# Optimization experiments

Hardware: AMD Instinct MI355X
Metric: run time of the kernel (lower is better)

The kernel has to match this reference:

```python
import jax, jax.numpy as jnp
import numpy as np
from jax import lax

NUM_CAMERAS = 15
INPUT_SIZE = 1024
NUM_TIMESTEPS = 60
BATCH = 256


def setup_inputs() -> dict:
    key = jax.random.key(0)
    k1, k2, k3, k4, k5, k6 = jax.random.split(key, 6)
    H = INPUT_SIZE
    s = 1.0 / np.sqrt(H)  # PyTorch RNNCell init: U(-1/sqrt(H), 1/sqrt(H))
    x = jax.random.normal(k1, (BATCH, H), dtype=jnp.float32)
    cam = jax.random.randint(k2, (BATCH,), 0, NUM_CAMERAS)
    # per-camera GRUCell params, PyTorch layout: gates [r, z, n] stacked -> 3H
    W_ih = jax.random.uniform(k3, (NUM_CAMERAS, 3 * H, H), jnp.float32, -s, s)
    W_hh = jax.random.uniform(k4, (NUM_CAMERAS, 3 * H, H), jnp.float32, -s, s)
    b_ih = jax.random.uniform(k5, (NUM_CAMERAS, 3 * H), jnp.float32, -s, s)
    b_hh = jax.random.uniform(k6, (NUM_CAMERAS, 3 * H), jnp.float32, -s, s)
    return {"x": x, "cam": cam, "W_ih": W_ih, "W_hh": W_hh, "b_ih": b_ih, "b_hh": b_hh}


def reference(x, cam, W_ih, W_hh, b_ih, b_hh):
    B, H = x.shape
    rows = jnp.arange(B)
    # input projection is constant across timesteps (same x fed every step):
    # compute for all cameras as one GEMM, then gather each sample's camera.
    gi_all = jnp.einsum('bh,cgh->bcg', x, W_ih) + b_ih[None]  # [B,C,3H]
    gi = gi_all[rows, cam]                                     # [B,3H]
    gi_r, gi_z, gi_n = jnp.split(gi, 3, axis=1)
    bhh = b_hh[cam]                                            # [B,3H]

    def step(h, _):
        gh_all = jnp.einsum('bh,cgh->bcg', h, W_hh)            # [B,C,3H] GEMM
        gh = gh_all[rows, cam] + bhh                           # [B,3H]
        gh_r, gh_z, gh_n = jnp.split(gh, 3, axis=1)
        r = jax.nn.sigmoid(gi_r + gh_r)
        z = jax.nn.sigmoid(gi_z + gh_z)
        n = jnp.tanh(gi_n + r * gh_n)
        h_new = (1.0 - z) * n + z * h
        return h_new, h_new

    h0 = jnp.zeros((B, H), dtype=x.dtype)
    _, hs = lax.scan(step, h0, None, length=NUM_TIMESTEPS)     # [T,B,H]
    return jnp.transpose(hs, (1, 2, 0))                        # [B,H,T]
```

## Files before the change

### kernel.cpp

```cpp
#include <hip/hip_runtime.h>
#include <math.h>

#define HD 1024
#define BB 256
#define NCAM 15
#define TT 60
#define G3 3072
#define LDW 36
#define NS 24
#define TCH 20

typedef short bf16x8 __attribute__((ext_vector_type(8)));
typedef _Float16 f16x8 __attribute__((ext_vector_type(8)));
typedef float f32x4 __attribute__((ext_vector_type(4)));

__device__ __forceinline__ unsigned short f2h(float f) {
    _Float16 h = (_Float16)f;
    unsigned short u;
    __builtin_memcpy(&u, &h, 2);
    return u;
}
__device__ __forceinline__ float sigf(float v) { return 1.f / (1.f + expf(-v)); }

__device__ __forceinline__ void dma16(const void* g, void* l) {
    __builtin_amdgcn_global_load_lds(
        (const __attribute__((address_space(1))) unsigned int*)g,
        (__attribute__((address_space(3))) unsigned int*)l, 16, 0, 0);
}

__global__ void group_kernel(const int* __restrict__ cam,
                             int* __restrict__ off, int* __restrict__ list) {
    __shared__ int cnt[NCAM];
    __shared__ int soff[NCAM + 1];
    int tid = threadIdx.x;
    if (tid < NCAM) cnt[tid] = 0;
    __syncthreads();
    int c = cam[tid];
    int pos = atomicAdd(&cnt[c], 1);
    __syncthreads();
    if (tid == 0) {
        soff[0] = 0;
        for (int i = 0; i < NCAM; ++i) soff[i + 1] = soff[i] + cnt[i];
    }
    __syncthreads();
    list[soff[c] + pos] = tid;
    if (tid <= NCAM) off[tid] = soff[tid];
}

__global__ __launch_bounds__(256) void gi_gemm_kernel(
    const float* __restrict__ W_ih, const float* __restrict__ b_ih,
    const float* __restrict__ b_hh, const float* __restrict__ x,
    const int* __restrict__ off, const int* __restrict__ list,
    float* __restrict__ gi) {
    int c  = blockIdx.x;
    int r0 = blockIdx.y * 96;
    int tid = threadIdx.x;
    int tx = tid & 7, ty = tid >> 3;

    __shared__ __align__(16) float wlds[96 * LDW];
    __shared__ __align__(16) float hlds[NS * LDW];
    __shared__ int slist[NS];

    int base = off[c];
    int nc = off[c + 1] - base;

    for (int s0 = 0; s0 < nc; s0 += NS) {
        __syncthreads();
        if (tid < NS) slist[tid] = (s0 + tid < nc) ? list[base + s0 + tid] : -1;
        __syncthreads();

        float acc[3][3];
#pragma unroll
        for (int g = 0; g < 3; ++g)
#pragma unroll
            for (int q = 0; q < 3; ++q) acc[g][q] = 0.f;

        for (int k0 = 0; k0 < HD; k0 += 32) {
#pragma unroll
            for (int i = 0; i < 3; ++i) {
                int idx = tid + 256 * i;
                int row = idx >> 3, col4 = idx & 7;
                float4 w = *(const float4*)(W_ih +
                    ((size_t)c * G3 + r0 + row) * HD + k0 + col4 * 4);
                *(float4*)(wlds + row * LDW + col4 * 4) = w;
            }
            {
                int s = tid >> 3, col4 = tid & 7;
                if (s < NS) {
                    int b = slist[s];
                    float4 hv = make_float4(0.f, 0.f, 0.f, 0.f);
                    if (b >= 0)
                        hv = *(const float4*)(x + (size_t)b * HD + k0 + col4 * 4);
                    *(float4*)(hlds + s * LDW + col4 * 4) = hv;
                }
            }
            __syncthreads();
#pragma unroll
            for (int kk = 0; kk < 32; kk += 4) {
                float4 w0 = *(const float4*)(wlds + (0 * 32 + ty) * LDW + kk);
                float4 w1 = *(const float4*)(wlds + (1 * 32 + ty) * LDW + kk);
                float4 w2 = *(const float4*)(wlds + (2 * 32 + ty) * LDW + kk);
#pragma unroll
                for (int q = 0; q < 3; ++q) {
                    float4 hv = *(const float4*)(hlds + (tx + 8 * q) * LDW + kk);
                    acc[0][q] += w0.x * hv.x + w0.y * hv.y + w0.z * hv.z + w0.w * hv.w;
                    acc[1][q] += w1.x * hv.x + w1.y * hv.y + w1.z * hv.z + w1.w * hv.w;
                    acc[2][q] += w2.x * hv.x + w2.y * hv.y + w2.z * hv.z + w2.w * hv.w;
                }
            }
            __syncthreads();
        }
#pragma unroll
        for (int q = 0; q < 3; ++q) {
            int b = slist[tx + 8 * q];
            if (b >= 0) {
#pragma unroll
                for (int g = 0; g < 3; ++g) {
                    int R = r0 + g * 32 + ty;
                    float bias = b_ih[c * G3 + R];
                    if (R < 2 * HD) bias += b_hh[c * G3 + R];
                    gi[(size_t)b * G3 + R] = acc[g][q] + bias;
                }
            }
        }
    }
}

__global__ __launch_bounds__(256) void prep_kernel(
    const float* __restrict__ W_hh, unsigned short* __restrict__ Wimg) {
    int c = blockIdx.z, jt = blockIdx.y;
    int lin = blockIdx.x * 256 + threadIdx.x;
    int it  = lin / 768;
    int rem = lin - it * 768;
    int r = rem >> 3, kcp = rem & 7;
    int gate = r >> 5, jl = r & 31;
    int kc = kcp ^ (r & 7);
    int k = it * 64 + kc * 8;
    const float* src = W_hh + ((size_t)c * G3 + gate * HD + jt * 32 + jl) * HD + k;
    float4 v0 = *(const float4*)src;
    float4 v1 = *(const float4*)(src + 4);
    float v[8] = {v0.x, v0.y, v0.z, v0.w, v1.x, v1.y, v1.z, v1.w};
    unsigned int hp[4];
#pragma unroll
    for (int e = 0; e < 4; ++e) {
        unsigned short h0 = f2h(v[2 * e]), h1 = f2h(v[2 * e + 1]);
        hp[e] = (unsigned)h0 | ((unsigned)h1 << 16);
    }
    unsigned short* dst = Wimg + ((size_t)(c * 32 + jt) * 16 + it) * 6144 + r * 64 + kcp * 8;
    *(uint4*)dst = make_uint4(hp[0], hp[1], hp[2], hp[3]);
}

__global__ __launch_bounds__(128) void step_dma_kernel(
    const unsigned short* __restrict__ Wimg, const float* __restrict__ b_hh,
    const float* __restrict__ gi, const int* __restrict__ off,
    const int* __restrict__ list, const float* __restrict__ h_in,
    const unsigned short* __restrict__ hf_in, const unsigned short* __restrict__ hzero,
    float* __restrict__ h_out, unsigned short* __restrict__ hf_out) {
    int c  = blockIdx.x;
    int jt = blockIdx.y;
    int j0 = jt * 32;
    int tid = threadIdx.x;
    int lane = tid & 63;
    int w = tid >> 6;
    int l15 = lane & 15;
    int l4  = lane >> 4;

    __shared__ __align__(16) unsigned short Ash[2][6144];
    __shared__ __align__(16) unsigned short Bsh[2][2048];
    __shared__ int slist[32];

    const unsigned short* wbase = Wimg + (size_t)(c * 32 + jt) * 16 * 6144;
    int base = off[c];
    int nc = off[c + 1] - base;

    int bs[2], bkc[2];
#pragma unroll
    for (int i = 0; i < 2; ++i) {
        int p = i * 128 + tid;
        bs[i]  = p >> 3;
        bkc[i] = (p & 7) ^ (bs[i] & 7);
    }

    for (int s0 = 0; s0 < nc; s0 += 32) {
        __syncthreads();
        if (tid < 32) slist[tid] = (s0 + tid < nc) ? list[base + s0 + tid] : -1;
        __syncthreads();
        int rem = nc - s0;
        int nq = (rem > 16) ? 2 : 1;

        const unsigned short* bg[2];
        int bstep[2];
#pragma unroll
        for (int i = 0; i < 2; ++i) {
            int b = slist[bs[i]];
            bg[i] = (b >= 0) ? hf_in + (size_t)b * HD + bkc[i] * 8 : hzero;
            bstep[i] = (b >= 0) ? 1 : 0;
        }

        f32x4 acc[3][2];
#pragma unroll
        for (int g = 0; g < 3; ++g)
#pragma unroll
            for (int q = 0; q < 2; ++q) acc[g][q] = (f32x4){0.f, 0.f, 0.f, 0.f};

#define STAGE(NB, IT) do {                                                        \
        const char* asrc_ = (const char*)(wbase + (size_t)(IT) * 6144);           \
        _Pragma("unroll")                                                         \
        for (int i_ = 0; i_ < 6; ++i_)                                            \
            dma16(asrc_ + (i_ * 128 + tid) * 16,                                  \
                  (char*)(Ash[NB]) + (i_ * 128 + (w << 6)) * 16);                 \
        int k0_ = (IT) * 64;                                                      \
        _Pragma("unroll")                                                         \
        for (int i_ = 0; i_ < 2; ++i_)                                            \
            dma16(bg[i_] + k0_ * bstep[i_],                                       \
                  (char*)(Bsh[NB]) + (i_ * 128 + (w << 6)) * 16);                 \
    } while (0)

        STAGE(0, 0);
        asm volatile("s_waitcnt vmcnt(0)" ::: "memory");
        __builtin_amdgcn_s_barrier();

#pragma unroll 2
        for (int it = 0; it < 16; ++it) {
            int cur = it & 1;
            if (it < 15) STAGE(cur ^ 1, it + 1);

            const unsigned short* Acur = Ash[cur];
            const unsigned short* Bcur = Bsh[cur];
#pragma unroll
            for (int kt = 0; kt < 2; ++kt) {
                int kc = kt * 4 + l4;
                f16x8 bq[2];
#pragma unroll
                for (int q = 0; q < 2; ++q) {
                    if (q < nq) {
                        int s = q * 16 + l15;
                        int boff = s * 64 + ((kc ^ (s & 7)) * 8);
                        bq[q] = *(const f16x8*)(&Bcur[boff]);
                    }
                }
#pragma unroll
                for (int g = 0; g < 3; ++g) {
                    int r = g * 32 + w * 16 + l15;
                    int aoff = r * 64 + ((kc ^ (r & 7)) * 8);
                    f16x8 av = *(const f16x8*)(&Acur[aoff]);
#pragma unroll
                    for (int q = 0; q < 2; ++q) {
                        if (q < nq) {
                            acc[g][q] = __builtin_amdgcn_mfma_f32_16x16x32_f16(av, bq[q], acc[g][q], 0, 0, 0);
                        }
                    }
                }
            }
            if (it < 15) {
                asm volatile("s_waitcnt vmcnt(0)" ::: "memory");
                __builtin_amdgcn_s_barrier();
            }
        }
#undef STAGE

        int j = j0 + w * 16 + l4 * 4;
        f32x4 bhn = *(const f32x4*)(b_hh + c * G3 + 2 * HD + j);
#pragma unroll
        for (int q = 0; q < 2; ++q) {
            if (q < nq) {
                int b = slist[q * 16 + l15];
                if (b >= 0) {
                    const float* gib = gi + (size_t)b * G3;
                    f32x4 gr = *(const f32x4*)(gib + j);
                    f32x4 gz = *(const f32x4*)(gib + HD + j);
                    f32x4 gn = *(const f32x4*)(gib + 2 * HD + j);
                    f32x4 hp = *(const f32x4*)(h_in + (size_t)b * HD + j);
                    f32x4 hn;
#pragma unroll
                    for (int e = 0; e < 4; ++e) {
                        float r = sigf(gr[e] + acc[0][q][e]);
                        float z = sigf(gz[e] + acc[1][q][e]);
                        float n = tanhf(gn[e] + r * (acc[2][q][e] + bhn[e]));
                        hn[e] = (1.f - z) * n + z * hp[e];
                    }
                    unsigned int hw[2];
#pragma unroll
                    for (int e = 0; e < 2; ++e) {
                        unsigned short h0 = f2h(hn[2 * e]), h1 = f2h(hn[2 * e + 1]);
                        hw[e] = (unsigned)h0 | ((unsigned)h1 << 16);
                    }
                    *(f32x4*)(h_out + (size_t)b * HD + j) = hn;
                    *(uint2*)(hf_out + (size_t)b * HD + j) = make_uint2(hw[0], hw[1]);
                }
            }
        }
    }
}

__global__ __launch_bounds__(256) void tr_kernel(
    const float* __restrict__ ring, float* __restrict__ out, int t0) {
    int r = blockIdx.x * 256 + threadIdx.x;
    float v[TCH];
#pragma unroll
    for (int tt = 0; tt < TCH; ++tt)
        v[tt] = ring[(size_t)tt * (BB * HD) + r];
    float* dst = out + (size_t)r * TT + t0;
#pragma unroll
    for (int e = 0; e < TCH / 4; ++e)
        *(f32x4*)(dst + 4 * e) = (f32x4){v[4 * e], v[4 * e + 1], v[4 * e + 2], v[4 * e + 3]};
}

extern "C" void kernel_launch(void* const* d_in, const int* in_sizes, int n_in,
                              void* d_out, int out_size, void* d_ws, size_t ws_size,
                              hipStream_t stream) {
    const float* x    = (const float*)d_in[0];
    const int*   cam  = (const int*)d_in[1];
    const float* W_ih = (const float*)d_in[2];
    const float* W_hh = (const float*)d_in[3];
    const float* b_ih = (const float*)d_in[4];
    const float* b_hh = (const float*)d_in[5];
    float* out = (float*)d_out;

    char* ws = (char*)d_ws;
    int*   off   = (int*)ws;
    int*   list  = (int*)(ws + 64);
    unsigned short* hzero = (unsigned short*)(ws + 2048);
    float* gi    = (float*)(ws + 4096);
    float* hZ    = (float*)(ws + 3149824);
    unsigned short* hfA = (unsigned short*)(ws + 4198400);
    unsigned short* hfB = (unsigned short*)(ws + 4722688);
    float* ring  = (float*)(ws + 5246976);
    unsigned short* Wimg = (unsigned short*)(ws + 26218496);

    group_kernel<<<1, 256, 0, stream>>>(cam, off, list);
    gi_gemm_kernel<<<dim3(NCAM, G3 / 96), 256, 0, stream>>>(
        W_ih, b_ih, b_hh, x, off, list, gi);
    prep_kernel<<<dim3(48, 32, NCAM), 256, 0, stream>>>(W_hh, Wimg);
    hipMemsetAsync(hzero, 0, 2048, stream);
    hipMemsetAsync(hZ, 0, (size_t)BB * HD * sizeof(float), stream);
    hipMemsetAsync(hfA, 0, (size_t)BB * HD * sizeof(short), stream);

    const float* hin = hZ;
    const unsigned short* hf_in = hfA;
    unsigned short* hf_out = hfB;
    for (int t = 0; t < TT; ++t) {
        float* ringplane = ring + (size_t)(t % TCH) * BB * HD;
        step_dma_kernel<<<dim3(NCAM, HD / 32), 128, 0, stream>>>(
            Wimg, b_hh, gi, off, list, hin, hf_in, hzero,
            ringplane, hf_out);
        hin = ringplane;
        { const unsigned short* tmp = hf_in; hf_in = hf_out; hf_out = (unsigned short*)tmp; }
        if ((t % TCH) == TCH - 1)
            tr_kernel<<<BB * HD / 256, 256, 0, stream>>>(ring, out, t - (TCH - 1));
    }
}
```

Baseline: 1.817 ms.

## Deepen step kernel DMA pipeline to four LDS stages with partial waits

The per-step GRU GEMM kernel moves from double-buffered LDS staging with a full vmcnt(0) drain each iteration to a 4-buffer ring with three tiles in flight. Each iteration waits only on the oldest tile's loads via partial vmcnt counts. The sample list is now kept in registers and broadcast with __shfl instead of going through shared memory, which removes one barrier per chunk. In exchange, LDS per block doubles, which may lower occupancy, and the hand-tuned vmcnt counts must exactly match the number of issued DMA ops.

Measured after the change: 1.743 ms. 1.04x faster.

```diff
diff --git a/kernel.cpp b/kernel.cpp
--- a/kernel.cpp
+++ b/kernel.cpp
@@ -10,7 +10,6 @@
 #define NS 24
 #define TCH 20
 
-typedef short bf16x8 __attribute__((ext_vector_type(8)));
 typedef _Float16 f16x8 __attribute__((ext_vector_type(8)));
 typedef float f32x4 __attribute__((ext_vector_type(4)));
 
@@ -165,9 +164,8 @@
     int l15 = lane & 15;
     int l4  = lane >> 4;
 
-    __shared__ __align__(16) unsigned short Ash[2][6144];
-    __shared__ __align__(16) unsigned short Bsh[2][2048];
-    __shared__ int slist[32];
+    __shared__ __align__(16) unsigned short Ash[4][6144];
+    __shared__ __align__(16) unsigned short Bsh[4][2048];
 
     const unsigned short* wbase = Wimg + (size_t)(c * 32 + jt) * 16 * 6144;
     int base = off[c];
@@ -181,10 +179,27 @@
         bkc[i] = (p & 7) ^ (bs[i] & 7);
     }
 
+#define STG_A(NB, IT) do {                                                    \
+        const char* asrc_ = (const char*)(wbase + (size_t)(IT) * 6144);       \
+        _Pragma("unroll")                                                     \
+        for (int i_ = 0; i_ < 6; ++i_)                                        \
+            dma16(asrc_ + (i_ * 128 + tid) * 16,                              \
+                  (char*)(Ash[NB]) + (i_ * 128 + (w << 6)) * 16);             \
+    } while (0)
+#define STG_B(NB, IT) do {                                                    \
+        int k0_ = (IT) * 64;                                                  \
+        _Pragma("unroll")                                                     \
+        for (int i_ = 0; i_ < 2; ++i_)                                        \
+            dma16(bg[i_] + k0_ * bstep[i_],                                   \
+                  (char*)(Bsh[NB]) + (i_ * 128 + (w << 6)) * 16);             \
+    } while (0)
+
     for (int s0 = 0; s0 < nc; s0 += 32) {
         __syncthreads();
-        if (tid < 32) slist[tid] = (s0 + tid < nc) ? list[base + s0 + tid] : -1;
-        __syncthreads();
+
+        int sv = -1;
+        if (lane < 32) sv = (s0 + lane < nc) ? list[base + s0 + lane] : -1;
+
         int rem = nc - s0;
         int nq = (rem > 16) ? 2 : 1;
 
@@ -192,7 +207,7 @@
         int bstep[2];
 #pragma unroll
         for (int i = 0; i < 2; ++i) {
-            int b = slist[bs[i]];
+            int b = __shfl(sv, bs[i]);
             bg[i] = (b >= 0) ? hf_in + (size_t)b * HD + bkc[i] * 8 : hzero;
             bstep[i] = (b >= 0) ? 1 : 0;
         }
@@ -203,30 +218,22 @@
 #pragma unroll
             for (int q = 0; q < 2; ++q) acc[g][q] = (f32x4){0.f, 0.f, 0.f, 0.f};
 
-#define STAGE(NB, IT) do {                                                        \
-        const char* asrc_ = (const char*)(wbase + (size_t)(IT) * 6144);           \
-        _Pragma("unroll")                                                         \
-        for (int i_ = 0; i_ < 6; ++i_)                                            \
-            dma16(asrc_ + (i_ * 128 + tid) * 16,                                  \
-                  (char*)(Ash[NB]) + (i_ * 128 + (w << 6)) * 16);                 \
-        int k0_ = (IT) * 64;                                                      \
-        _Pragma("unroll")                                                         \
-        for (int i_ = 0; i_ < 2; ++i_)                                            \
-            dma16(bg[i_] + k0_ * bstep[i_],                                       \
-                  (char*)(Bsh[NB]) + (i_ * 128 + (w << 6)) * 16);                 \
-    } while (0)
-
-        STAGE(0, 0);
         asm volatile("s_waitcnt vmcnt(0)" ::: "memory");
-        __builtin_amdgcn_s_barrier();
-
-#pragma unroll 2
+
+        STG_A(0, 0); STG_B(0, 0);
+        STG_A(1, 1); STG_B(1, 1);
+        STG_A(2, 2); STG_B(2, 2);
+
+#pragma unroll
         for (int it = 0; it < 16; ++it) {
-            int cur = it & 1;
-            if (it < 15) STAGE(cur ^ 1, it + 1);
-
-            const unsigned short* Acur = Ash[cur];
-            const unsigned short* Bcur = Bsh[cur];
+            if (it < 14)       asm volatile("s_waitcnt vmcnt(16)" ::: "memory");
+            else if (it == 14) asm volatile("s_waitcnt vmcnt(8)"  ::: "memory");
+            else               asm volatile("s_waitcnt vmcnt(0)"  ::: "memory");
+            __builtin_amdgcn_s_barrier();
+            if (it < 13) { STG_A((it + 3) & 3, it + 3); STG_B((it + 3) & 3, it + 3); }
+
+            const unsigned short* Acur = Ash[it & 3];
+            const unsigned short* Bcur = Bsh[it & 3];
 #pragma unroll
             for (int kt = 0; kt < 2; ++kt) {
                 int kc = kt * 4 + l4;
@@ -252,19 +259,14 @@
                     }
                 }
             }
-            if (it < 15) {
-                asm volatile("s_waitcnt vmcnt(0)" ::: "memory");
-                __builtin_amdgcn_s_barrier();
-            }
-        }
-#undef STAGE
+        }
 
         int j = j0 + w * 16 + l4 * 4;
         f32x4 bhn = *(const f32x4*)(b_hh + c * G3 + 2 * HD + j);
 #pragma unroll
         for (int q = 0; q < 2; ++q) {
             if (q < nq) {
-                int b = slist[q * 16 + l15];
+                int b = __shfl(sv, q * 16 + l15);
                 if (b >= 0) {
                     const float* gib = gi + (size_t)b * G3;
                     f32x4 gr = *(const f32x4*)(gib + j);
@@ -291,6 +293,8 @@
             }
         }
     }
+#undef STG_A
+#undef STG_B
 }
 
 __global__ __launch_bounds__(256) void tr_kernel(
```
